# Kernel optimization log

Measured on AMD Instinct MI355X. Metric: run time of the kernel, lower is better.

The kernel has to match this reference:

```python
import jax, jax.numpy as jnp
import numpy as np

D_MODEL = 1024
D_FF = 2048
N_EXPERTS = 8
TOP_K = 2


def setup_inputs() -> dict:
    key = jax.random.key(0)
    ks = jax.random.split(key, 10)
    s = 0.02
    return {
        "x": jax.random.normal(ks[0], (2, 1024, D_MODEL), dtype=jnp.float32),
        "gate_w": jax.random.normal(ks[1], (N_EXPERTS, D_MODEL), dtype=jnp.float32) * s,
        "gate_b": jnp.zeros((N_EXPERTS,), jnp.float32),
        "Wg": jax.random.normal(ks[2], (N_EXPERTS, D_MODEL, D_FF), dtype=jnp.float32) * s,
        "bg": jnp.zeros((N_EXPERTS, D_FF), jnp.float32),
        "Wu": jax.random.normal(ks[3], (N_EXPERTS, D_MODEL, D_FF), dtype=jnp.float32) * s,
        "bu": jnp.zeros((N_EXPERTS, D_FF), jnp.float32),
        "Wd": jax.random.normal(ks[4], (N_EXPERTS, D_FF, D_MODEL), dtype=jnp.float32) * s,
        "bd": jnp.zeros((N_EXPERTS, D_MODEL), jnp.float32),
    }


def reference(x, gate_w, gate_b, Wg, bg, Wu, bu, Wd, bd):
    b, s, d = x.shape
    xf = x.reshape(-1, d)                       # (T, d)
    T = xf.shape[0]
    # --- router ---
    logits = xf @ gate_w.T + gate_b             # (T, E)
    probs = jax.nn.softmax(logits.astype(jnp.float32), axis=-1)
    # load-balance loss: KL(ideal || mean_probs), reduction='sum'
    expert_probs = probs.mean(axis=0)
    ideal = 1.0 / N_EXPERTS
    balance_loss = jnp.sum(ideal * (jnp.log(ideal) - jnp.log(expert_probs + 1e-9)))
    # top-k routing, renormalized
    vals, idx = jax.lax.top_k(probs, TOP_K)     # (T, K)
    w = vals / vals.sum(axis=-1, keepdims=True)
    # per-token per-expert combine weight (T, E); zero for non-selected experts
    cw = jnp.zeros((T, N_EXPERTS), jnp.float32).at[
        jnp.arange(T)[:, None], idx].add(w)
    # --- experts (SwiGLU MLP), batched over E, masked combine ---
    g = jnp.einsum('td,edf->tef', xf, Wg) + bg[None]   # (T, E, F)
    u = jnp.einsum('td,edf->tef', xf, Wu) + bu[None]
    h = jax.nn.silu(g) * u
    out = jnp.einsum('tef,efd->ted', h, Wd) + bd[None]  # (T, E, d)
    y = jnp.einsum('ted,te->td', out, cw.astype(x.dtype))
    return y.reshape(b, s, d), balance_loss
```

## Files before the change

### kernel.cpp

```cpp
#include <hip/hip_runtime.h>
#include <hip/hip_bf16.h>


#define D_MODEL 1024
#define D_FF    2048
#define N_EXP   8
#define T_TOK   2048
#define MAXTILES 40

typedef __attribute__((ext_vector_type(8))) short bf16x8;
typedef __attribute__((ext_vector_type(8))) ushort u16x8;
typedef __attribute__((ext_vector_type(4))) float f32x4;

__device__ __forceinline__ ushort f2bf(float f) {
    union { float f; unsigned u; } c; c.f = f;
    unsigned u = c.u;
    return (ushort)((u + 0x7fffu + ((u >> 16) & 1u)) >> 16);
}

__device__ __forceinline__ void glds16(const void* g, void* l) {
    __builtin_amdgcn_global_load_lds(
        (const __attribute__((address_space(1))) unsigned int*)g,
        (__attribute__((address_space(3))) unsigned int*)l, 16, 0, 0);
}

__global__ __launch_bounds__(256) void k_prep_w(
    const float* __restrict__ Wg, const float* __restrict__ Wu, const float* __restrict__ Wd,
    ushort* __restrict__ Wgt, ushort* __restrict__ Wut, ushort* __restrict__ Wdt)
{
    int t = blockIdx.x;
    int which = blockIdx.y;
    const float* src; ushort* dst; int N, nt, kt;
    int e = t >> 8;
    if (which == 2) { src = Wd; dst = Wdt; N = 1024; nt = (t >> 5) & 7;  kt = t & 31; }
    else            { src = (which ? Wu : Wg); dst = (which ? Wut : Wgt); N = 2048; nt = (t >> 4) & 15; kt = t & 15; }

    int tid = threadIdx.x;
    int kb = tid >> 5;
    int c4 = (tid & 31) * 4;
    size_t K = (N == 2048) ? 1024 : 2048;
    const float* p = src + (size_t)e * K * N + (size_t)(kt * 64 + kb * 8) * N + nt * 128 + c4;

    float4 v[8];
#pragma unroll
    for (int j = 0; j < 8; j++)
        v[j] = *(const float4*)(p + (size_t)j * N);

    u16x8 o0, o1, o2, o3;
#pragma unroll
    for (int j = 0; j < 8; j++) {
        o0[j] = f2bf(v[j].x);
        o1[j] = f2bf(v[j].y);
        o2[j] = f2bf(v[j].z);
        o3[j] = f2bf(v[j].w);
    }
    ushort* d = dst + (size_t)t * 8192 + (size_t)(kb * 128 + c4) * 8;
    *(u16x8*)(d + 0)  = o0;
    *(u16x8*)(d + 8)  = o1;
    *(u16x8*)(d + 16) = o2;
    *(u16x8*)(d + 24) = o3;
}

__global__ __launch_bounds__(256) void k_router(
    const float* __restrict__ x, const float* __restrict__ gw, const float* __restrict__ gb,
    int* cnt, float* probsum, int* tok, int* slotpk, float* wtok,
    ushort* __restrict__ xb)
{
    __shared__ float gws[N_EXP * D_MODEL];
    __shared__ float ps_s[N_EXP];
    __shared__ int   bc_s[N_EXP];
    __shared__ int   gb_s[N_EXP];
    __shared__ int   a_e[64];
    __shared__ int   a_lp[64];

    int tid = threadIdx.x;
    for (int i = tid; i < N_EXP * D_MODEL / 4; i += 256)
        ((float4*)gws)[i] = ((const float4*)gw)[i];
    if (tid < N_EXP) { ps_s[tid] = 0.f; bc_s[tid] = 0; }
    __syncthreads();

    int wave = tid >> 6, lane = tid & 63;

    for (int it = 0; it < 8; it++) {
        int tb = it * 4 + wave;
        int t = blockIdx.x * 32 + tb;
        const float4* xr = (const float4*)(x + (size_t)t * D_MODEL);
        ushort* xbr = xb + (size_t)t * D_MODEL;

        float acc[N_EXP];
#pragma unroll
        for (int e = 0; e < N_EXP; e++) acc[e] = 0.f;
#pragma unroll
        for (int q = 0; q < 4; q++) {
            int idx = q * 64 + lane;
            float4 xv = xr[idx];
            ushort4 xc;
            xc.x = f2bf(xv.x); xc.y = f2bf(xv.y); xc.z = f2bf(xv.z); xc.w = f2bf(xv.w);
            *(ushort4*)&xbr[idx * 4] = xc;
#pragma unroll
            for (int e = 0; e < N_EXP; e++) {
                float4 gv = ((const float4*)(gws + e * D_MODEL))[idx];
                acc[e] += xv.x * gv.x + xv.y * gv.y + xv.z * gv.z + xv.w * gv.w;
            }
        }
#pragma unroll
        for (int off = 32; off > 0; off >>= 1) {
#pragma unroll
            for (int e = 0; e < N_EXP; e++) acc[e] += __shfl_xor(acc[e], off, 64);
        }
        if (lane == 0) {
            float l[N_EXP], m = -1e30f;
#pragma unroll
            for (int e = 0; e < N_EXP; e++) { l[e] = acc[e] + gb[e]; m = fmaxf(m, l[e]); }
            float p[N_EXP], s = 0.f;
#pragma unroll
            for (int e = 0; e < N_EXP; e++) { p[e] = expf(l[e] - m); s += p[e]; }
            float inv = 1.f / s;
#pragma unroll
            for (int e = 0; e < N_EXP; e++) { p[e] *= inv; atomicAdd(&ps_s[e], p[e]); }
            int i0 = 0; float v0 = p[0];
#pragma unroll
            for (int e = 1; e < N_EXP; e++) if (p[e] > v0) { v0 = p[e]; i0 = e; }
            int i1 = -1; float v1 = -1.f;
#pragma unroll
            for (int e = 0; e < N_EXP; e++) if (e != i0 && p[e] > v1) { v1 = p[e]; i1 = e; }
            float winv = 1.f / (v0 + v1);
            int lp0 = atomicAdd(&bc_s[i0], 1);
            int lp1 = atomicAdd(&bc_s[i1], 1);
            a_e[tb * 2 + 0] = i0; a_lp[tb * 2 + 0] = lp0;
            a_e[tb * 2 + 1] = i1; a_lp[tb * 2 + 1] = lp1;
            wtok[t * 2 + 0] = v0 * winv;
            wtok[t * 2 + 1] = v1 * winv;
        }
    }
    __syncthreads();
    if (tid < N_EXP) {
        gb_s[tid] = atomicAdd(&cnt[tid], bc_s[tid]);
        atomicAdd(&probsum[tid], ps_s[tid]);
    }
    __syncthreads();
    if (tid < 64) {
        int tb = tid >> 1, k = tid & 1;
        int t = blockIdx.x * 32 + tb;
        int e = a_e[tid];
        int slot = gb_s[e] + a_lp[tid];
        tok[e * T_TOK + slot] = t;
        slotpk[t * 2 + k] = (e << 16) | slot;
    }
}

__global__ void k_base_loss(const int* __restrict__ cnt, const float* __restrict__ probsum,
                            int* abase, int* tile, float* loss_out)
{
    if (threadIdx.x == 0 && blockIdx.x == 0) {
        int b = 0, nt = 0;
        float loss = 0.f;
        for (int e = 0; e < N_EXP; e++) {
            abase[e] = b;
            for (int m0 = 0; m0 < cnt[e]; m0 += 128)
                tile[nt++] = (e << 16) | m0;
            b += ((cnt[e] + 127) >> 7) * 128;
            float mean = probsum[e] * (1.0f / T_TOK);
            loss += 0.125f * (logf(0.125f) - logf(mean + 1e-9f));
        }
        for (; nt < MAXTILES; nt++) tile[nt] = -1;
        *loss_out = loss;
    }
}

__global__ __launch_bounds__(256, 2) void k_expert_gu(
    const ushort* __restrict__ Wgt, const ushort* __restrict__ Wut,
    const float* __restrict__ bg, const float* __restrict__ bu,
    const ushort* __restrict__ xb, const int* __restrict__ cnt,
    const int* __restrict__ abase, const int* __restrict__ tile,
    const int* __restrict__ tok, ushort* __restrict__ h_t)
{
    int ti = tile[blockIdx.x];
    if (ti < 0) return;
    int e = ti >> 16, m0 = ti & 0xffff;
    int ne = cnt[e];
    int nt = blockIdx.y;
    int n0 = nt * 128;
    int stile = (abase[e] >> 7) + (m0 >> 7);

    __shared__ __align__(16) ushort As[128 * 88];
    __shared__ __align__(16) ushort Bg_s[8192];
    __shared__ __align__(16) ushort Bu_s[8192];

    int tid = threadIdx.x;
    int lane = tid & 63, wave = tid >> 6;
    int wm = (wave & 1) * 64, wn = (wave >> 1) * 64;

    int arow = tid >> 1;
    int akh = (tid & 1) * 32;
    int atok = tok[e * T_TOK + min(m0 + arow, ne - 1)];
    const ushort* xrow = xb + (size_t)atok * D_MODEL;

    const char* gbase = (const char*)(Wgt + (size_t)(e * 16 + nt) * 16 * 8192);
    const char* ubase = (const char*)(Wut + (size_t)(e * 16 + nt) * 16 * 8192);
    int goff = tid * 16;
    int loff = (tid >> 6) * 1024;

    f32x4 accg[4][4], accu[4][4];
#pragma unroll
    for (int i = 0; i < 4; i++)
#pragma unroll
        for (int j = 0; j < 4; j++) {
            accg[i][j] = (f32x4){0.f, 0.f, 0.f, 0.f};
            accu[i][j] = (f32x4){0.f, 0.f, 0.f, 0.f};
        }

    for (int kt = 0; kt < D_MODEL / 64; kt++) {
        __syncthreads();
#pragma unroll
        for (int q = 0; q < 4; q++)
            *(uint4*)&As[arow * 88 + akh + q * 8] = *(const uint4*)&xrow[kt * 64 + akh + q * 8];
        const char* gsrc = gbase + kt * 16384;
        const char* usrc = ubase + kt * 16384;
#pragma unroll
        for (int q = 0; q < 4; q++) {
            glds16(gsrc + q * 4096 + goff, (char*)Bg_s + q * 4096 + loff);
            glds16(usrc + q * 4096 + goff, (char*)Bu_s + q * 4096 + loff);
        }
        __syncthreads();
#pragma unroll
        for (int ks = 0; ks < 2; ks++) {
            bf16x8 af[4];
            int arow_f = wm + (lane & 15);
            int akb = ks * 32 + (lane >> 4) * 8;
#pragma unroll
            for (int sm = 0; sm < 4; sm++)
                af[sm] = *(const bf16x8*)&As[(arow_f + sm * 16) * 88 + akb];
            int bkb = ks * 4 + (lane >> 4);
#pragma unroll
            for (int sn = 0; sn < 4; sn++) {
                int ncol = wn + sn * 16 + (lane & 15);
                bf16x8 bgf = *(const bf16x8*)&Bg_s[(bkb * 128 + ncol) * 8];
                bf16x8 buf = *(const bf16x8*)&Bu_s[(bkb * 128 + ncol) * 8];
#pragma unroll
                for (int sm = 0; sm < 4; sm++) {
                    accg[sm][sn] = __builtin_amdgcn_mfma_f32_16x16x32_bf16(af[sm], bgf, accg[sm][sn], 0, 0, 0);
                    accu[sm][sn] = __builtin_amdgcn_mfma_f32_16x16x32_bf16(af[sm], buf, accu[sm][sn], 0, 0, 0);
                }
            }
        }
    }
    int rbase = wm + ((lane >> 4) << 2);
    int cbase = wn + (lane & 15);
    size_t tbase = (size_t)stile * 32 * 8192;
#pragma unroll
    for (int sm = 0; sm < 4; sm++) {
#pragma unroll
        for (int r = 0; r < 4; r++) {
            int pos = m0 + rbase + sm * 16 + r;
            if (pos < ne) {
                int row = pos & 127;
#pragma unroll
                for (int sn = 0; sn < 4; sn++) {
                    int col = n0 + cbase + sn * 16;
                    float g = accg[sm][sn][r] + bg[e * D_FF + col];
                    float u = accu[sm][sn][r] + bu[e * D_FF + col];
                    float hv = (g / (1.f + expf(-g))) * u;
                    int ktb = col >> 6, kb = (col >> 3) & 7, ko = col & 7;
                    h_t[tbase + (size_t)ktb * 8192 + (kb * 128 + row) * 8 + ko] = f2bf(hv);
                }
            }
        }
    }
}

__global__ __launch_bounds__(256, 2) void k_expert_down(
    const ushort* __restrict__ Wdt, const float* __restrict__ bd,
    const ushort* __restrict__ h_t, const int* __restrict__ cnt,
    const int* __restrict__ abase, const int* __restrict__ tile,
    float* __restrict__ outp)
{
    int ti = tile[blockIdx.x];
    if (ti < 0) return;
    int e = ti >> 16, m0 = ti & 0xffff;
    int ne = cnt[e];
    int nt = blockIdx.y;
    int n0 = nt * 128;
    int stile = (abase[e] >> 7) + (m0 >> 7);

    __shared__ __align__(16) ushort As8[8192];
    __shared__ __align__(16) ushort Bd_s[8192];

    int tid = threadIdx.x;
    int lane = tid & 63, wave = tid >> 6;
    int wm = (wave & 1) * 64, wn = (wave >> 1) * 64;

    const char* hbase = (const char*)(h_t + (size_t)stile * 32 * 8192);
    const char* dbase = (const char*)(Wdt + (size_t)(e * 8 + nt) * 32 * 8192);
    int goff = tid * 16;
    int loff = (tid >> 6) * 1024;

    f32x4 acc[4][4];
#pragma unroll
    for (int i = 0; i < 4; i++)
#pragma unroll
        for (int j = 0; j < 4; j++) acc[i][j] = (f32x4){0.f, 0.f, 0.f, 0.f};

    for (int kt = 0; kt < D_FF / 64; kt++) {
        __syncthreads();
        const char* asrc = hbase + kt * 16384;
        const char* bsrc = dbase + kt * 16384;
#pragma unroll
        for (int q = 0; q < 4; q++) {
            glds16(asrc + q * 4096 + goff, (char*)As8 + q * 4096 + loff);
            glds16(bsrc + q * 4096 + goff, (char*)Bd_s + q * 4096 + loff);
        }
        __syncthreads();
#pragma unroll
        for (int ks = 0; ks < 2; ks++) {
            bf16x8 af[4];
            int kb = ks * 4 + (lane >> 4);
            int arow_f = wm + (lane & 15);
#pragma unroll
            for (int sm = 0; sm < 4; sm++)
                af[sm] = *(const bf16x8*)&As8[(kb * 128 + arow_f + sm * 16) * 8];
#pragma unroll
            for (int sn = 0; sn < 4; sn++) {
                int ncol = wn + sn * 16 + (lane & 15);
                bf16x8 bdf = *(const bf16x8*)&Bd_s[(kb * 128 + ncol) * 8];
#pragma unroll
                for (int sm = 0; sm < 4; sm++)
                    acc[sm][sn] = __builtin_amdgcn_mfma_f32_16x16x32_bf16(af[sm], bdf, acc[sm][sn], 0, 0, 0);
            }
        }
    }
    int rbase = wm + ((lane >> 4) << 2);
    int cbase = wn + (lane & 15);
#pragma unroll
    for (int sm = 0; sm < 4; sm++) {
#pragma unroll
        for (int r = 0; r < 4; r++) {
            int pos = m0 + rbase + sm * 16 + r;
            if (pos < ne) {
                size_t ob = (size_t)(abase[e] + pos) * D_MODEL;
#pragma unroll
                for (int sn = 0; sn < 4; sn++) {
                    int col = n0 + cbase + sn * 16;
                    outp[ob + col] = acc[sm][sn][r] + bd[e * D_MODEL + col];
                }
            }
        }
    }
}

__global__ void k_combine(const float* __restrict__ outp, const int* __restrict__ slotpk,
                          const float* __restrict__ wtok, const int* __restrict__ abase,
                          float* __restrict__ y)
{
    int idx = blockIdx.x * 256 + threadIdx.x;
    int t = idx >> 8, j = idx & 255;
    int sp0 = slotpk[t * 2 + 0], sp1 = slotpk[t * 2 + 1];
    float w0 = wtok[t * 2 + 0], w1 = wtok[t * 2 + 1];
    size_t s0 = (size_t)abase[sp0 >> 16] + (sp0 & 0xffff);
    size_t s1 = (size_t)abase[sp1 >> 16] + (sp1 & 0xffff);
    float4 a = ((const float4*)outp)[s0 * (D_MODEL / 4) + j];
    float4 b = ((const float4*)outp)[s1 * (D_MODEL / 4) + j];
    float4 o;
    o.x = w0 * a.x + w1 * b.x;
    o.y = w0 * a.y + w1 * b.y;
    o.z = w0 * a.z + w1 * b.z;
    o.w = w0 * a.w + w1 * b.w;
    ((float4*)y)[idx] = o;
}

extern "C" void kernel_launch(void* const* d_in, const int* in_sizes, int n_in,
                              void* d_out, int out_size, void* d_ws, size_t ws_size,
                              hipStream_t stream)
{
    const float* x  = (const float*)d_in[0];
    const float* gw = (const float*)d_in[1];
    const float* gb = (const float*)d_in[2];
    const float* Wg = (const float*)d_in[3];
    const float* bg = (const float*)d_in[4];
    const float* Wu = (const float*)d_in[5];
    const float* bu = (const float*)d_in[6];
    const float* Wd = (const float*)d_in[7];
    const float* bd = (const float*)d_in[8];
    float* y = (float*)d_out;
    float* loss_out = y + (size_t)T_TOK * D_MODEL;

    char* ws = (char*)d_ws;
    int*    cnt     = (int*)(ws + 0);
    float*  probsum = (float*)(ws + 128);
    int*    abase   = (int*)(ws + 256);
    int*    tiletab = (int*)(ws + 320);
    int*    slotpk  = (int*)(ws + 512);
    float*  wtok    = (float*)(ws + 16896);
    int*    tok     = (int*)(ws + 33280);
    ushort* xb      = (ushort*)(ws + 131072);
    ushort* Wgt     = (ushort*)(ws + 4325376);
    ushort* Wut     = (ushort*)(ws + 37879808);
    ushort* Wdt     = (ushort*)(ws + 71434240);
    ushort* h_t     = (ushort*)(ws + 104988672);
    float*  outp    = (float*)(ws + 125960192);

    hipMemsetAsync(d_ws, 0, 256, stream);
    k_prep_w<<<dim3(2048, 3), dim3(256), 0, stream>>>(Wg, Wu, Wd, Wgt, Wut, Wdt);
    k_router<<<dim3(64), dim3(256), 0, stream>>>(x, gw, gb, cnt, probsum, tok, slotpk, wtok, xb);
    k_base_loss<<<dim3(1), dim3(64), 0, stream>>>(cnt, probsum, abase, tiletab, loss_out);
    k_expert_gu<<<dim3(MAXTILES, 16), dim3(256), 0, stream>>>(Wgt, Wut, bg, bu, xb, cnt, abase, tiletab, tok, h_t);
    k_expert_down<<<dim3(MAXTILES, 8), dim3(256), 0, stream>>>(Wdt, bd, h_t, cnt, abase, tiletab, outp);
    k_combine<<<dim3(2048), dim3(256), 0, stream>>>(outp, slotpk, wtok, abase, y);
}
```

Before: 383.7 us.

## Stage weight bf16 conversion through LDS for contiguous global reads and writes

Rewrites the weight fp32-to-bf16 repacking kernel so each block reads a contiguous 64KB slab of rows with fully coalesced float4 loads. It converts into LDS, transposes 8x8 chunks in registers, and writes back through a swizzled LDS layout so the global stores are contiguous 16-byte chunks. The aim is to replace the previous strided row reads with streaming access in this bandwidth-bound prep pass. The cost is halving the grid, adding 32KB of LDS per block and three barriers.

```diff
diff --git a/kernel.cpp b/kernel.cpp
--- a/kernel.cpp
+++ b/kernel.cpp
@@ -28,37 +28,75 @@
     const float* __restrict__ Wg, const float* __restrict__ Wu, const float* __restrict__ Wd,
     ushort* __restrict__ Wgt, ushort* __restrict__ Wut, ushort* __restrict__ Wdt)
 {
-    int t = blockIdx.x;
+    __shared__ __align__(16) ushort lds[16384];
+
+    int s = blockIdx.x;
     int which = blockIdx.y;
-    const float* src; ushort* dst; int N, nt, kt;
-    int e = t >> 8;
-    if (which == 2) { src = Wd; dst = Wdt; N = 1024; nt = (t >> 5) & 7;  kt = t & 31; }
-    else            { src = (which ? Wu : Wg); dst = (which ? Wut : Wgt); N = 2048; nt = (t >> 4) & 15; kt = t & 15; }
-
     int tid = threadIdx.x;
-    int kb = tid >> 5;
-    int c4 = (tid & 31) * 4;
-    size_t K = (N == 2048) ? 1024 : 2048;
-    const float* p = src + (size_t)e * K * N + (size_t)(kt * 64 + kb * 8) * N + nt * 128 + c4;
-
-    float4 v[8];
+    int e = s >> 7;
+
+    const float* src; ushort* dst;
+    int kt, kb, kbp;
+    size_t soff;
+    if (which == 2) {
+        src = Wd; dst = Wdt;
+        kt = (s >> 2) & 31; kbp = s & 3; kb = 0;
+        soff = (size_t)e * 2048 * 1024 + (size_t)(kt * 64 + kbp * 16) * 1024;
+    } else {
+        src = which ? Wu : Wg; dst = which ? Wut : Wgt;
+        kt = (s >> 3) & 15; kb = s & 7; kbp = 0;
+        soff = (size_t)e * 1024 * 2048 + (size_t)(kt * 64 + kb * 8) * 2048;
+    }
+    const float4* p = (const float4*)(src + soff);
+
+#pragma unroll
+    for (int i = 0; i < 16; i++) {
+        float4 v = p[i * 256 + tid];
+        ushort4 o;
+        o.x = f2bf(v.x); o.y = f2bf(v.y); o.z = f2bf(v.z); o.w = f2bf(v.w);
+        *(ushort4*)&lds[(i * 256 + tid) * 4] = o;
+    }
+    __syncthreads();
+
+    u16x8 in[8];
+    if (which == 2) {
+        int th = tid >> 7, tc = tid & 127;
+#pragma unroll
+        for (int ko = 0; ko < 8; ko++)
+            in[ko] = *(const u16x8*)&lds[(th * 8 + ko) * 1024 + tc * 8];
+    } else {
+#pragma unroll
+        for (int ko = 0; ko < 8; ko++)
+            in[ko] = *(const u16x8*)&lds[ko * 2048 + tid * 8];
+    }
+    u16x8 out[8];
 #pragma unroll
     for (int j = 0; j < 8; j++)
-        v[j] = *(const float4*)(p + (size_t)j * N);
-
-    u16x8 o0, o1, o2, o3;
-#pragma unroll
-    for (int j = 0; j < 8; j++) {
-        o0[j] = f2bf(v[j].x);
-        o1[j] = f2bf(v[j].y);
-        o2[j] = f2bf(v[j].z);
-        o3[j] = f2bf(v[j].w);
-    }
-    ushort* d = dst + (size_t)t * 8192 + (size_t)(kb * 128 + c4) * 8;
-    *(u16x8*)(d + 0)  = o0;
-    *(u16x8*)(d + 8)  = o1;
-    *(u16x8*)(d + 16) = o2;
-    *(u16x8*)(d + 24) = o3;
+#pragma unroll
+        for (int ko = 0; ko < 8; ko++)
+            out[j][ko] = in[ko][j];
+    __syncthreads();
+
+    int swz = (tid & 7) << 4;
+#pragma unroll
+    for (int j = 0; j < 8; j++)
+        *(u16x8*)((char*)lds + ((((8 * tid + j) * 16) ^ swz))) = out[j];
+    __syncthreads();
+
+#pragma unroll
+    for (int i = 0; i < 8; i++) {
+        int c = i * 256 + tid;
+        u16x8 v = *(const u16x8*)((char*)lds + ((c * 16) ^ (((c >> 3) & 7) << 4)));
+        int R = c >> 7, q = c & 127;
+        size_t gaddr;
+        if (which == 2) {
+            int kb2 = R >> 3, ntp = R & 7;
+            gaddr = (size_t)(e * 256 + ntp * 32 + kt) * 8192 + (kbp * 2 + kb2) * 1024 + q * 8;
+        } else {
+            gaddr = (size_t)(e * 256 + R * 16 + kt) * 8192 + kb * 1024 + q * 8;
+        }
+        *(u16x8*)&dst[gaddr] = v;
+    }
 }
 
 __global__ __launch_bounds__(256) void k_router(
@@ -400,7 +438,7 @@
     float*  outp    = (float*)(ws + 125960192);
 
     hipMemsetAsync(d_ws, 0, 256, stream);
-    k_prep_w<<<dim3(2048, 3), dim3(256), 0, stream>>>(Wg, Wu, Wd, Wgt, Wut, Wdt);
+    k_prep_w<<<dim3(1024, 3), dim3(256), 0, stream>>>(Wg, Wu, Wd, Wgt, Wut, Wdt);
     k_router<<<dim3(64), dim3(256), 0, stream>>>(x, gw, gb, cnt, probsum, tok, slotpk, wtok, xb);
     k_base_loss<<<dim3(1), dim3(64), 0, stream>>>(cnt, probsum, abase, tiletab, loss_out);
     k_expert_gu<<<dim3(MAXTILES, 16), dim3(256), 0, stream>>>(Wgt, Wut, bg, bu, xb, cnt, abase, tiletab, tok, h_t);
```

Result: no change. 386.9 us (+0.8%).

## Fuse fp32-to-bf16 weight conversion into expert GEMMs with register prefetch

Applied to the files above, without the earlier changes.

Drops the separate weight pre-conversion kernel. The gate/up and down GEMMs now load fp32 weights straight from global memory, convert them to bf16 in registers and store them into shared memory. Loads for the next k-tile are issued before the MFMA loop, a register double-buffering scheme that replaces the async global_load_lds path. This saves writing and re-reading about 100MB of bf16 weights each call. In exchange, each weight tile is read as fp32 once per token tile (up to roughly 40 times), with more conversion ALU work and higher register pressure at 2 blocks per CU.

```diff
diff --git a/kernel.cpp b/kernel.cpp
--- a/kernel.cpp
+++ b/kernel.cpp
@@ -16,49 +16,6 @@
     union { float f; unsigned u; } c; c.f = f;
     unsigned u = c.u;
     return (ushort)((u + 0x7fffu + ((u >> 16) & 1u)) >> 16);
-}
-
-__device__ __forceinline__ void glds16(const void* g, void* l) {
-    __builtin_amdgcn_global_load_lds(
-        (const __attribute__((address_space(1))) unsigned int*)g,
-        (__attribute__((address_space(3))) unsigned int*)l, 16, 0, 0);
-}
-
-__global__ __launch_bounds__(256) void k_prep_w(
-    const float* __restrict__ Wg, const float* __restrict__ Wu, const float* __restrict__ Wd,
-    ushort* __restrict__ Wgt, ushort* __restrict__ Wut, ushort* __restrict__ Wdt)
-{
-    int t = blockIdx.x;
-    int which = blockIdx.y;
-    const float* src; ushort* dst; int N, nt, kt;
-    int e = t >> 8;
-    if (which == 2) { src = Wd; dst = Wdt; N = 1024; nt = (t >> 5) & 7;  kt = t & 31; }
-    else            { src = (which ? Wu : Wg); dst = (which ? Wut : Wgt); N = 2048; nt = (t >> 4) & 15; kt = t & 15; }
-
-    int tid = threadIdx.x;
-    int kb = tid >> 5;
-    int c4 = (tid & 31) * 4;
-    size_t K = (N == 2048) ? 1024 : 2048;
-    const float* p = src + (size_t)e * K * N + (size_t)(kt * 64 + kb * 8) * N + nt * 128 + c4;
-
-    float4 v[8];
-#pragma unroll
-    for (int j = 0; j < 8; j++)
-        v[j] = *(const float4*)(p + (size_t)j * N);
-
-    u16x8 o0, o1, o2, o3;
-#pragma unroll
-    for (int j = 0; j < 8; j++) {
-        o0[j] = f2bf(v[j].x);
-        o1[j] = f2bf(v[j].y);
-        o2[j] = f2bf(v[j].z);
-        o3[j] = f2bf(v[j].w);
-    }
-    ushort* d = dst + (size_t)t * 8192 + (size_t)(kb * 128 + c4) * 8;
-    *(u16x8*)(d + 0)  = o0;
-    *(u16x8*)(d + 8)  = o1;
-    *(u16x8*)(d + 16) = o2;
-    *(u16x8*)(d + 24) = o3;
 }
 
 __global__ __launch_bounds__(256) void k_router(
@@ -169,7 +126,7 @@
 }
 
 __global__ __launch_bounds__(256, 2) void k_expert_gu(
-    const ushort* __restrict__ Wgt, const ushort* __restrict__ Wut,
+    const float* __restrict__ Wg, const float* __restrict__ Wu,
     const float* __restrict__ bg, const float* __restrict__ bu,
     const ushort* __restrict__ xb, const int* __restrict__ cnt,
     const int* __restrict__ abase, const int* __restrict__ tile,
@@ -196,10 +153,12 @@
     int atok = tok[e * T_TOK + min(m0 + arow, ne - 1)];
     const ushort* xrow = xb + (size_t)atok * D_MODEL;
 
-    const char* gbase = (const char*)(Wgt + (size_t)(e * 16 + nt) * 16 * 8192);
-    const char* ubase = (const char*)(Wut + (size_t)(e * 16 + nt) * 16 * 8192);
-    int goff = tid * 16;
-    int loff = (tid >> 6) * 1024;
+    int skb = tid >> 5;
+    int sc4 = (tid & 31) * 4;
+    const float* gp = Wg + (size_t)e * D_MODEL * D_FF + (size_t)(skb * 8) * D_FF + n0 + sc4;
+    const float* up = Wu + (size_t)e * D_MODEL * D_FF + (size_t)(skb * 8) * D_FF + n0 + sc4;
+    ushort* dgs = Bg_s + (skb * 128 + sc4) * 8;
+    ushort* dus = Bu_s + (skb * 128 + sc4) * 8;
 
     f32x4 accg[4][4], accu[4][4];
 #pragma unroll
@@ -210,17 +169,36 @@
             accu[i][j] = (f32x4){0.f, 0.f, 0.f, 0.f};
         }
 
+    float4 vg[8], vu[8];
+#pragma unroll
+    for (int j = 0; j < 8; j++) {
+        vg[j] = *(const float4*)(gp + (size_t)j * D_FF);
+        vu[j] = *(const float4*)(up + (size_t)j * D_FF);
+    }
+
     for (int kt = 0; kt < D_MODEL / 64; kt++) {
         __syncthreads();
 #pragma unroll
         for (int q = 0; q < 4; q++)
             *(uint4*)&As[arow * 88 + akh + q * 8] = *(const uint4*)&xrow[kt * 64 + akh + q * 8];
-        const char* gsrc = gbase + kt * 16384;
-        const char* usrc = ubase + kt * 16384;
-#pragma unroll
-        for (int q = 0; q < 4; q++) {
-            glds16(gsrc + q * 4096 + goff, (char*)Bg_s + q * 4096 + loff);
-            glds16(usrc + q * 4096 + goff, (char*)Bu_s + q * 4096 + loff);
+        u16x8 g0, g1, g2, g3, u0, u1, u2, u3;
+#pragma unroll
+        for (int j = 0; j < 8; j++) {
+            g0[j] = f2bf(vg[j].x); g1[j] = f2bf(vg[j].y); g2[j] = f2bf(vg[j].z); g3[j] = f2bf(vg[j].w);
+            u0[j] = f2bf(vu[j].x); u1[j] = f2bf(vu[j].y); u2[j] = f2bf(vu[j].z); u3[j] = f2bf(vu[j].w);
+        }
+        *(u16x8*)(dgs + 0)  = g0; *(u16x8*)(dgs + 8)  = g1;
+        *(u16x8*)(dgs + 16) = g2; *(u16x8*)(dgs + 24) = g3;
+        *(u16x8*)(dus + 0)  = u0; *(u16x8*)(dus + 8)  = u1;
+        *(u16x8*)(dus + 16) = u2; *(u16x8*)(dus + 24) = u3;
+        if (kt < D_MODEL / 64 - 1) {
+            const float* gn = gp + (size_t)(kt + 1) * 64 * D_FF;
+            const float* un = up + (size_t)(kt + 1) * 64 * D_FF;
+#pragma unroll
+            for (int j = 0; j < 8; j++) {
+                vg[j] = *(const float4*)(gn + (size_t)j * D_FF);
+                vu[j] = *(const float4*)(un + (size_t)j * D_FF);
+            }
         }
         __syncthreads();
 #pragma unroll
@@ -270,7 +248,7 @@
 }
 
 __global__ __launch_bounds__(256, 2) void k_expert_down(
-    const ushort* __restrict__ Wdt, const float* __restrict__ bd,
+    const float* __restrict__ Wd, const float* __restrict__ bd,
     const ushort* __restrict__ h_t, const int* __restrict__ cnt,
     const int* __restrict__ abase, const int* __restrict__ tile,
     float* __restrict__ outp)
@@ -290,25 +268,43 @@
     int lane = tid & 63, wave = tid >> 6;
     int wm = (wave & 1) * 64, wn = (wave >> 1) * 64;
 
-    const char* hbase = (const char*)(h_t + (size_t)stile * 32 * 8192);
-    const char* dbase = (const char*)(Wdt + (size_t)(e * 8 + nt) * 32 * 8192);
-    int goff = tid * 16;
-    int loff = (tid >> 6) * 1024;
+    const uint4* hbase = (const uint4*)(h_t + (size_t)stile * 32 * 8192);
+
+    int skb = tid >> 5, sc4 = (tid & 31) * 4;
+    const float* dp = Wd + (size_t)e * D_FF * D_MODEL + (size_t)(skb * 8) * D_MODEL + n0 + sc4;
+    ushort* dds = Bd_s + (skb * 128 + sc4) * 8;
 
     f32x4 acc[4][4];
 #pragma unroll
     for (int i = 0; i < 4; i++)
 #pragma unroll
         for (int j = 0; j < 4; j++) acc[i][j] = (f32x4){0.f, 0.f, 0.f, 0.f};
+
+    uint4 va[4];
+    float4 vd[8];
+#pragma unroll
+    for (int q = 0; q < 4; q++) va[q] = hbase[q * 256 + tid];
+#pragma unroll
+    for (int j = 0; j < 8; j++) vd[j] = *(const float4*)(dp + (size_t)j * D_MODEL);
 
     for (int kt = 0; kt < D_FF / 64; kt++) {
         __syncthreads();
-        const char* asrc = hbase + kt * 16384;
-        const char* bsrc = dbase + kt * 16384;
-#pragma unroll
-        for (int q = 0; q < 4; q++) {
-            glds16(asrc + q * 4096 + goff, (char*)As8 + q * 4096 + loff);
-            glds16(bsrc + q * 4096 + goff, (char*)Bd_s + q * 4096 + loff);
+#pragma unroll
+        for (int q = 0; q < 4; q++) ((uint4*)As8)[q * 256 + tid] = va[q];
+        u16x8 d0, d1, d2, d3;
+#pragma unroll
+        for (int j = 0; j < 8; j++) {
+            d0[j] = f2bf(vd[j].x); d1[j] = f2bf(vd[j].y); d2[j] = f2bf(vd[j].z); d3[j] = f2bf(vd[j].w);
+        }
+        *(u16x8*)(dds + 0)  = d0; *(u16x8*)(dds + 8)  = d1;
+        *(u16x8*)(dds + 16) = d2; *(u16x8*)(dds + 24) = d3;
+        if (kt < D_FF / 64 - 1) {
+            const uint4* hn = hbase + (kt + 1) * 1024;
+            const float* dn = dp + (size_t)(kt + 1) * 64 * D_MODEL;
+#pragma unroll
+            for (int q = 0; q < 4; q++) va[q] = hn[q * 256 + tid];
+#pragma unroll
+            for (int j = 0; j < 8; j++) vd[j] = *(const float4*)(dn + (size_t)j * D_MODEL);
         }
         __syncthreads();
 #pragma unroll
@@ -393,17 +389,13 @@
     float*  wtok    = (float*)(ws + 16896);
     int*    tok     = (int*)(ws + 33280);
     ushort* xb      = (ushort*)(ws + 131072);
-    ushort* Wgt     = (ushort*)(ws + 4325376);
-    ushort* Wut     = (ushort*)(ws + 37879808);
-    ushort* Wdt     = (ushort*)(ws + 71434240);
-    ushort* h_t     = (ushort*)(ws + 104988672);
-    float*  outp    = (float*)(ws + 125960192);
-
-    hipMemsetAsync(d_ws, 0, 256, stream);
-    k_prep_w<<<dim3(2048, 3), dim3(256), 0, stream>>>(Wg, Wu, Wd, Wgt, Wut, Wdt);
+    ushort* h_t     = (ushort*)(ws + 4325376);
+    float*  outp    = (float*)(ws + 25296896);
+
+    (void)hipMemsetAsync(d_ws, 0, 256, stream);
     k_router<<<dim3(64), dim3(256), 0, stream>>>(x, gw, gb, cnt, probsum, tok, slotpk, wtok, xb);
     k_base_loss<<<dim3(1), dim3(64), 0, stream>>>(cnt, probsum, abase, tiletab, loss_out);
-    k_expert_gu<<<dim3(MAXTILES, 16), dim3(256), 0, stream>>>(Wgt, Wut, bg, bu, xb, cnt, abase, tiletab, tok, h_t);
-    k_expert_down<<<dim3(MAXTILES, 8), dim3(256), 0, stream>>>(Wdt, bd, h_t, cnt, abase, tiletab, outp);
+    k_expert_gu<<<dim3(MAXTILES, 16), dim3(256), 0, stream>>>(Wg, Wu, bg, bu, xb, cnt, abase, tiletab, tok, h_t);
+    k_expert_down<<<dim3(MAXTILES, 8), dim3(256), 0, stream>>>(Wd, bd, h_t, cnt, abase, tiletab, outp);
     k_combine<<<dim3(2048), dim3(256), 0, stream>>>(outp, slotpk, wtok, abase, y);
 }
```

New measurement: 453.4 us. 18.2% more time.
